# Optimization experiments

Hardware: AMD Instinct MI355X
Metric: run time of the kernel (lower is better)

## Reference

```python
import jax, jax.numpy as jnp
import numpy as np

B, N, C = 4, 1024, 512
H = 8
HD = C // H
SCALE = HD ** (-0.5)


def setup_inputs() -> dict:
    key = jax.random.key(0)
    ks = jax.random.split(key, 12)
    s = 0.02
    return {
        "x": jax.random.normal(ks[0], (B, N, C), dtype=jnp.float32),
        "y": jax.random.normal(ks[1], (B, N, C), dtype=jnp.float32),
        "Wqkv1": jax.random.normal(ks[2], (4 * C, C), dtype=jnp.float32) * s,
        "Wqkv2": jax.random.normal(ks[3], (4 * C, C), dtype=jnp.float32) * s,
        "W1": jax.random.normal(ks[4], (C, C), dtype=jnp.float32) * s,
        "b1": jnp.zeros((C,), dtype=jnp.float32),
        "W2": jax.random.normal(ks[5], (C, C), dtype=jnp.float32) * s,
        "b2": jnp.zeros((C,), dtype=jnp.float32),
        "W3": jax.random.normal(ks[6], (C, C), dtype=jnp.float32) * s,
        "b3": jnp.zeros((C,), dtype=jnp.float32),
        "W4": jax.random.normal(ks[7], (C, C), dtype=jnp.float32) * s,
        "b4": jnp.zeros((C,), dtype=jnp.float32),
    }


def _l2norm(t, eps=1e-12):
    # matches F.normalize(dim=-1)
    n = jnp.sqrt(jnp.sum(t * t, axis=-1, keepdims=True))
    return t / jnp.maximum(n, eps)


def _ortho_loss(q, qt):
    # q, qt: [B, H, N, HD]
    qn = _l2norm(q)
    qtn = _l2norm(qt)
    prod = jnp.einsum("bhnd,bhmd->bhnm", qn, qtn)  # [B,H,N,N]
    eye = jnp.eye(N, dtype=prod.dtype)
    off = prod * (1.0 - eye)
    # fro-norm squared of off-diagonal, divided by B*N*N (as in source)
    return jnp.sum(off * off) / (B * N * N)


def _qkv(inp, W):
    # inp: [B,N,C], W: [4C, C] -> [4, B, H, N, HD]
    t = (inp @ W.T).reshape(B, N, 4, H, HD)
    return jnp.transpose(t, (2, 0, 3, 1, 4))


def _attn(q, k, v):
    # q,k,v: [B,H,N,HD] -> [B,N,C]
    scores = jnp.einsum("bhnd,bhmd->bhnm", q, k) * SCALE
    a = jax.nn.softmax(scores, axis=-1)
    o = jnp.einsum("bhnm,bhmd->bhnd", a, v)
    return jnp.transpose(o, (0, 2, 1, 3)).reshape(B, N, C)


def reference(x, y, Wqkv1, Wqkv2, W1, b1, W2, b2, W3, b3, W4, b4):
    qkv1 = _qkv(x, Wqkv1)
    qkv2 = _qkv(y, Wqkv2)
    qx, kx, vx, qtx = qkv1[0], qkv1[1], qkv1[2], qkv1[3]
    qy, ky, vy, qty = qkv2[0], qkv2[1], qkv2[2], qkv2[3]

    lorthx = _ortho_loss(qx, qtx)
    lorthy = _ortho_loss(qy, qty)

    yc = _attn(qx, ky, vy)  # attncy @ vy
    xc = _attn(qy, kx, vx)  # attncx @ vx
    xt = _attn(qtx, kx, vx)
    yt = _attn(qty, ky, vy)

    xc = xc @ W1.T + b1
    yc = yc @ W2.T + b2
    xt = xt @ W3.T + b3
    yt = yt @ W4.T + b4

    # pairwise cosine distance between normalized xc, yc
    xcn = _l2norm(xc)
    ycn = _l2norm(yc)
    cos = jnp.sum(xcn * ycn, axis=-1)
    lc = jnp.mean(1.0 - cos)

    return (xc, yc, xt, yt, lorthx, lorthy, lc)
```

## Files before the change

### kernel.cpp

```cpp
#include <hip/hip_runtime.h>

typedef unsigned short u16;
typedef __attribute__((ext_vector_type(4))) unsigned short u16x4;
typedef __attribute__((ext_vector_type(8))) unsigned short u16x8;
typedef __attribute__((ext_vector_type(4))) float          f32x4;
typedef __attribute__((ext_vector_type(8))) __bf16         bf16x8;

#define MFMA16(a,b,c) __builtin_amdgcn_mfma_f32_16x16x32_bf16((a),(b),(c),0,0,0)
#define SCALE 0.125f
#define SCALE_LOG2E 0.18033688011112042f

__device__ __forceinline__ u16 f2b(float f){
  unsigned u = __builtin_bit_cast(unsigned, f);
  u = (u + 0x7fffu + ((u >> 16) & 1u)) >> 16;
  return (u16)u;
}
__device__ __forceinline__ u16 f2b_trunc(float f){
  return (u16)(__builtin_bit_cast(unsigned, f) >> 16);
}
__device__ __forceinline__ float b2f(u16 v){
  unsigned u = ((unsigned)v) << 16;
  return __builtin_bit_cast(float, u);
}
__device__ __forceinline__ void async16(const u16* g, u16* l){
  __builtin_amdgcn_global_load_lds(
      (const __attribute__((address_space(1))) unsigned*)g,
      (__attribute__((address_space(3))) unsigned*)l, 16, 0, 0);
}
__device__ __forceinline__ int swz(int row, int chunk, int off){
  return row*64 + (((chunk ^ row ^ (row >> 3)) & 7) << 3) + off;
}

__global__ void cast_all_k(const float* __restrict__ x, const float* __restrict__ y,
                           const float* __restrict__ wq1, const float* __restrict__ wq2,
                           const float* __restrict__ w1, const float* __restrict__ w2,
                           const float* __restrict__ w3, const float* __restrict__ w4,
                           u16* __restrict__ dst, float* __restrict__ outs){
  if (blockIdx.x == 0 && threadIdx.x < 3) outs[threadIdx.x] = 0.f;
  int i = blockIdx.x * 256 + threadIdx.x;
  const float* s; int base; float sc = 1.f;
  if      (i < 524288)  { s = x;   base = 0;       }
  else if (i < 1048576) { s = y;   base = 524288;  }
  else if (i < 1310720) { s = wq1; base = 1048576;
    int iw = i - base; if (iw < 65536 || iw >= 196608) sc = SCALE_LOG2E; }
  else if (i < 1572864) { s = wq2; base = 1310720;
    int iw = i - base; if (iw < 65536 || iw >= 196608) sc = SCALE_LOG2E; }
  else if (i < 1638400) { s = w1;  base = 1572864; }
  else if (i < 1703936) { s = w2;  base = 1638400; }
  else if (i < 1769472) { s = w3;  base = 1703936; }
  else                  { s = w4;  base = 1769472; }
  float4 v = ((const float4*)s)[i - base];
  u16x4 o; o[0]=f2b(v.x*sc); o[1]=f2b(v.y*sc); o[2]=f2b(v.z*sc); o[3]=f2b(v.w*sc);
  ((u16x4*)dst)[i] = o;
}

__global__ __launch_bounds__(256, 2) void qkv_mega_k(
    const u16* __restrict__ xb, const u16* __restrict__ Wq,
    u16* __restrict__ qkv, u16* __restrict__ vT)
{
  const int i = blockIdx.x;
  const u16 *A, *B; u16* C; int ldc, m0, n0;
  if (i < 512) {
    int z = i >> 8, t = i & 255;
    m0 = (t & 31)*128; n0 = (t >> 5)*128;
    A = xb + (size_t)z*2097152; B = Wq + (size_t)z*1048576;
    C = qkv + (size_t)z*8388608; ldc = 2048;
  } else if (i < 768) {
    int z = (i-512) >> 7, t = (i-512) & 127;
    m0 = (t & 31)*128; n0 = (t >> 5)*128;
    A = xb + (size_t)z*2097152; B = Wq + (size_t)z*1048576 + (size_t)1536*512;
    C = qkv + (size_t)z*8388608 + 1536; ldc = 2048;
  } else {
    int z = (i-768) >> 7, t = (i-768) & 127;
    m0 = (t & 3)*128; n0 = (t >> 2)*128;
    A = Wq + (size_t)z*1048576 + (size_t)1024*512; B = xb + (size_t)z*2097152;
    C = vT + (size_t)z*2097152; ldc = 4096;
  }

  __shared__ u16 As[128*32];
  __shared__ u16 Bs[128*32];
  const int tid  = threadIdx.x;
  const int w    = tid >> 6, lane = tid & 63;
  const int quad = lane >> 4, l16 = lane & 15;
  const int wr   = w >> 1, wc = w & 1;

  f32x4 acc[4][4] = {};
  const int rowa = lane >> 2;
  const int ko   = (lane & 3) * 8;

  for (int k0 = 0; k0 < 512; k0 += 32) {
    __syncthreads();
#pragma unroll
    for (int r = 0; r < 2; ++r) {
      int rb = (r*4 + w) * 16;
      async16(A + (size_t)(m0 + rb + rowa)*512 + k0 + ko, As + (r*4 + w)*512);
      async16(B + (size_t)(n0 + rb + rowa)*512 + k0 + ko, Bs + (r*4 + w)*512);
    }
    __syncthreads();
    bf16x8 af[4], bfr[4];
#pragma unroll
    for (int ii = 0; ii < 4; ++ii)
      af[ii] = *(const bf16x8*)&As[(wr*64 + ii*16 + l16)*32 + quad*8];
#pragma unroll
    for (int j = 0; j < 4; ++j)
      bfr[j] = *(const bf16x8*)&Bs[(wc*64 + j*16 + l16)*32 + quad*8];
#pragma unroll
    for (int ii = 0; ii < 4; ++ii)
#pragma unroll
      for (int j = 0; j < 4; ++j)
        acc[ii][j] = MFMA16(af[ii], bfr[j], acc[ii][j]);
  }
#pragma unroll
  for (int j = 0; j < 4; ++j) {
    int col = n0 + wc*64 + j*16 + l16;
#pragma unroll
    for (int ii = 0; ii < 4; ++ii)
#pragma unroll
      for (int reg = 0; reg < 4; ++reg) {
        int row = m0 + wr*64 + ii*16 + quad*4 + reg;
        C[(size_t)row*ldc + col] = f2b(acc[ii][j][reg]);
      }
  }
}

__global__ __launch_bounds__(256, 2) void gemm_fin_k(
    const u16* __restrict__ A0, size_t aStr, const u16* __restrict__ B0, size_t bStr,
    const float* __restrict__ bias0, const float* __restrict__ bias1,
    const float* __restrict__ bias2, const float* __restrict__ bias3,
    float* __restrict__ C0, size_t cStr,
    const float* __restrict__ Gbuf, float* __restrict__ outs)
{
  const int tid  = threadIdx.x;
  const int bid  = blockIdx.x;
  if (bid >= 512) {
    const int i = bid - 512;
    const int bh = i & 31, which = i >> 5;
    const float* base = Gbuf + (size_t)((which*32 + bh)*8) * 8192;
    float acc = 0.f;
    for (int idx = tid*4; idx < 4096; idx += 1024) {
      float4 gq = {0.f,0.f,0.f,0.f}, gt = {0.f,0.f,0.f,0.f};
#pragma unroll
      for (int t = 0; t < 8; ++t) {
        float4 a = *(const float4*)(base + (size_t)t*8192 + idx);
        float4 c = *(const float4*)(base + (size_t)t*8192 + 4096 + idx);
        gq.x += a.x; gq.y += a.y; gq.z += a.z; gq.w += a.w;
        gt.x += c.x; gt.y += c.y; gt.z += c.z; gt.w += c.w;
      }
      acc += gq.x*gt.x + gq.y*gt.y + gq.z*gt.z + gq.w*gt.w;
    }
    __shared__ float redsh[256];
    redsh[tid] = acc; __syncthreads();
    for (int s2 = 128; s2 > 0; s2 >>= 1) {
      if (tid < s2) redsh[tid] += redsh[tid + s2];
      __syncthreads();
    }
    if (tid == 0) atomicAdd(&outs[which], redsh[0] * (1.f/4194304.f));
    return;
  }

  const int z = bid >> 7, t7 = bid & 127;
  const int m0 = (t7 >> 2) * 128, n0 = (t7 & 3) * 128;
  const u16* A = A0 + (size_t)z * aStr;
  const u16* Bm = B0 + (size_t)z * bStr;
  float* Cb = C0 + (size_t)z * cStr;
  const float* bias = (z==0) ? bias0 : (z==1) ? bias1 : (z==2) ? bias2 : bias3;

  __shared__ u16 As[128*32];
  __shared__ u16 Bs[128*32];
  const int w    = tid >> 6, lane = tid & 63;
  const int quad = lane >> 4, l16 = lane & 15;
  const int wr   = w >> 1, wc = w & 1;

  f32x4 acc[4][4] = {};
  const int rowa = lane >> 2;
  const int ko   = (lane & 3) * 8;

  for (int k0 = 0; k0 < 512; k0 += 32) {
    __syncthreads();
#pragma unroll
    for (int r = 0; r < 2; ++r) {
      int rb = (r*4 + w) * 16;
      async16(A  + (size_t)(m0 + rb + rowa)*512 + k0 + ko, As + (r*4 + w)*512);
      async16(Bm + (size_t)(n0 + rb + rowa)*512 + k0 + ko, Bs + (r*4 + w)*512);
    }
    __syncthreads();
    bf16x8 af[4], bfr[4];
#pragma unroll
    for (int ii = 0; ii < 4; ++ii)
      af[ii] = *(const bf16x8*)&As[(wr*64 + ii*16 + l16)*32 + quad*8];
#pragma unroll
    for (int j = 0; j < 4; ++j)
      bfr[j] = *(const bf16x8*)&Bs[(wc*64 + j*16 + l16)*32 + quad*8];
#pragma unroll
    for (int ii = 0; ii < 4; ++ii)
#pragma unroll
      for (int j = 0; j < 4; ++j)
        acc[ii][j] = MFMA16(af[ii], bfr[j], acc[ii][j]);
  }
#pragma unroll
  for (int j = 0; j < 4; ++j) {
    int col = n0 + wc*64 + j*16 + l16;
    float bv = bias[col];
#pragma unroll
    for (int ii = 0; ii < 4; ++ii)
#pragma unroll
      for (int reg = 0; reg < 4; ++reg) {
        int row = m0 + wr*64 + ii*16 + quad*4 + reg;
        Cb[(size_t)row*512 + col] = acc[ii][j][reg] + bv;
      }
  }
}

__global__ __launch_bounds__(256, 2) void attn_ortho_k(
    const u16* __restrict__ qkv1, const u16* __restrict__ qkv2,
    const u16* __restrict__ vT1, const u16* __restrict__ vT2,
    u16* __restrict__ ao, float* __restrict__ Gbuf, float* __restrict__ outs)
{
  __shared__ u16 lds[24576];
  const int tid = threadIdx.x, w = tid >> 6, lane = tid & 63;
  const int quad = lane >> 4, l16 = lane & 15;

  if (blockIdx.x < 512) {
    u16* Ks = lds;
    u16* Vt = lds + 8192;
    u16* Ps = lds + 16384;

    const int lin = blockIdx.x;
    const int xcd = lin & 7, slot = lin >> 3;
    const int g   = xcd + 8*(slot >> 3);
    const int qt  = slot & 7;
    const int bh  = g >> 1, p = g & 1;
    const int b = bh >> 3, h = bh & 7;
    const u16* kvsrc = p ? qkv2 : qkv1;
    const u16* vsrc  = p ? vT2 : vT1;
    const u16* qsrcA = p ? qkv1 : qkv2;  const int qoffA = h*64;
    const u16* qsrcB = p ? qkv2 : qkv1;  const int qoffB = 1536 + h*64;
    const int koff = 512 + h*64;
    const size_t tb = (size_t)b * 1024;

    const int srow = tid >> 3, sch = tid & 7;

    u16x8 onesu;
#pragma unroll
    for (int ii = 0; ii < 8; ++ii) onesu[ii] = 0x3f80;
    const bf16x8 ONES = __builtin_bit_cast(bf16x8, onesu);

    bf16x8 qb[2][2][2];
#pragma unroll
    for (int s2 = 0; s2 < 2; ++s2) {
      size_t row = tb + qt*128 + w*32 + s2*16 + l16;
      const u16* qrA = qsrcA + row*2048 + qoffA;
      const u16* qrB = qsrcB + row*2048 + qoffB;
      qb[0][s2][0] = *(const bf16x8*)(qrA + quad*8);
      qb[0][s2][1] = *(const bf16x8*)(qrA + 32 + quad*8);
      qb[1][s2][0] = *(const bf16x8*)(qrB + quad*8);
      qb[1][s2][1] = *(const bf16x8*)(qrB + 32 + quad*8);
    }

    f32x4 oacc[2][2][4] = {};
    f32x4 lacc[2][2] = {};

    u16x8 kreg[2], vreg[2];
    auto loadTile = [&](int t){
#pragma unroll
      for (int r = 0; r < 2; ++r) {
        kreg[r] = *(const u16x8*)(kvsrc + (tb + t*64 + r*32 + srow)*2048 + koff + sch*8);
        vreg[r] = *(const u16x8*)(vsrc + (size_t)(h*64 + r*32 + srow)*4096 + tb + t*64 + sch*8);
      }
    };
    auto storeTile = [&](int buf){
#pragma unroll
      for (int r = 0; r < 2; ++r) {
        *(u16x8*)&Ks[buf*4096 + swz(r*32 + srow, sch, 0)] = kreg[r];
        *(u16x8*)&Vt[buf*4096 + swz(r*32 + srow, sch, 0)] = vreg[r];
      }
    };

    loadTile(0);
    storeTile(0);
    loadTile(1);

    for (int kt = 0; kt < 16; ++kt) {
      const int cur = kt & 1;
      __syncthreads();
      if (kt < 15) storeTile(cur ^ 1);
      if (kt < 14) loadTile(kt + 2);

      bf16x8 ka[4][2], vb[4][2];
#pragma unroll
      for (int j = 0; j < 4; ++j) {
        ka[j][0] = *(const bf16x8*)&Ks[cur*4096 + swz(j*16 + l16, quad, 0)];
        ka[j][1] = *(const bf16x8*)&Ks[cur*4096 + swz(j*16 + l16, quad + 4, 0)];
        vb[j][0] = *(const bf16x8*)&Vt[cur*4096 + swz(j*16 + l16, quad, 0)];
        vb[j][1] = *(const bf16x8*)&Vt[cur*4096 + swz(j*16 + l16, quad + 4, 0)];
      }

      bf16x8 paP0, paP1;
#pragma unroll
      for (int idx = 0; idx < 4; ++idx) {
        const int o = idx >> 1, s2 = idx & 1;
        u16* wP = Ps + w*2048 + (idx & 1)*1024;
        f32x4 t[4];
        __builtin_amdgcn_s_setprio(1);
#pragma unroll
        for (int j = 0; j < 4; ++j) {
          f32x4 z = {};
          z    = MFMA16(ka[j][0], qb[o][s2][0], z);
          t[j] = MFMA16(ka[j][1], qb[o][s2][1], z);
        }
        __builtin_amdgcn_s_setprio(0);
        if (idx > 0) {
          const u16* rP = Ps + w*2048 + ((idx - 1) & 1)*1024;
          paP0 = *(const bf16x8*)&rP[swz(l16, quad, 0)];
          paP1 = *(const bf16x8*)&rP[swz(l16, quad + 4, 0)];
        }
#pragma unroll
        for (int j = 0; j < 4; ++j) {
          u16x4 pk;
#pragma unroll
          for (int reg = 0; reg < 4; ++reg)
            pk[reg] = f2b_trunc(__builtin_amdgcn_exp2f(t[j][reg]));
          *(u16x4*)&wP[swz(l16, j*2 + (quad >> 1), (quad & 1)*4)] = pk;
        }
        if (idx > 0) {
          const int po = (idx - 1) >> 1, ps2 = (idx - 1) & 1;
          __builtin_amdgcn_s_setprio(1);
#pragma unroll
          for (int j = 0; j < 4; ++j) {
            oacc[po][ps2][j] = MFMA16(paP0, vb[j][0], oacc[po][ps2][j]);
            oacc[po][ps2][j] = MFMA16(paP1, vb[j][1], oacc[po][ps2][j]);
          }
          lacc[po][ps2] = MFMA16(paP0, ONES, lacc[po][ps2]);
          lacc[po][ps2] = MFMA16(paP1, ONES, lacc[po][ps2]);
          __builtin_amdgcn_s_setprio(0);
        }
      }
      {
        const u16* rP = Ps + w*2048 + 1024;
        bf16x8 pa0 = *(const bf16x8*)&rP[swz(l16, quad, 0)];
        bf16x8 pa1 = *(const bf16x8*)&rP[swz(l16, quad + 4, 0)];
        __builtin_amdgcn_s_setprio(1);
#pragma unroll
        for (int j = 0; j < 4; ++j) {
          oacc[1][1][j] = MFMA16(pa0, vb[j][0], oacc[1][1][j]);
          oacc[1][1][j] = MFMA16(pa1, vb[j][1], oacc[1][1][j]);
        }
        lacc[1][1] = MFMA16(pa0, ONES, lacc[1][1]);
        lacc[1][1] = MFMA16(pa1, ONES, lacc[1][1]);
        __builtin_amdgcn_s_setprio(0);
      }
    }

#pragma unroll
    for (int o = 0; o < 2; ++o) {
      int a = p + o*2;
      u16* aop = ao + (size_t)a*(4096*512) + (tb + qt*128)*512 + h*64;
#pragma unroll
      for (int s2 = 0; s2 < 2; ++s2) {
#pragma unroll
        for (int reg = 0; reg < 4; ++reg) {
          float linv = 1.f / lacc[o][s2][reg];
          int row = w*32 + s2*16 + quad*4 + reg;
#pragma unroll
          for (int j = 0; j < 4; ++j)
            aop[(size_t)row*512 + j*16 + l16] = f2b(oacc[o][s2][j][reg] * linv);
        }
      }
    }
  } else {
    u16* QnT  = lds;
    u16* QtnT = lds + 4096;

    const int i = blockIdx.x - 512;
    const int bh = i & 31, which = (i >> 5) & 1, tg = i >> 6;
    const u16* src = which ? qkv2 : qkv1;
    const int b = bh >> 3, h = bh & 7;
    const size_t tb = (size_t)b * 1024;

    f32x4 gq[4] = {}, gqt[4] = {};
    float diag = 0.f;

    for (int tt = 0; tt < 2; ++tt) {
      int t = tg*2 + tt;
      __syncthreads();
      if (tid < 128) {
        int tok = tid & 63, mat = tid >> 6;
        const u16* pp = src + (tb + t*64 + tok)*2048 + (mat ? 1536 : 0) + h*64;
        u16x8 rowv[8];
#pragma unroll
        for (int ii = 0; ii < 8; ++ii) rowv[ii] = *(const u16x8*)(pp + ii*8);
        float ss = 0.f;
#pragma unroll
        for (int ii = 0; ii < 8; ++ii)
#pragma unroll
          for (int jj = 0; jj < 8; ++jj) { float f = b2f(rowv[ii][jj]); ss += f*f; }
        float inv = 1.f / fmaxf(sqrtf(ss), 1e-12f);
        u16* dst = mat ? QtnT : QnT;
#pragma unroll
        for (int ii = 0; ii < 8; ++ii)
#pragma unroll
          for (int jj = 0; jj < 8; ++jj)
            dst[swz(ii*8 + jj, tok >> 3, tok & 7)] = f2b(b2f(rowv[ii][jj]) * inv);
        if (mat == 0) {
          const u16* p2 = src + (tb + t*64 + tok)*2048 + 1536 + h*64;
          float ss2 = 0.f, dot = 0.f;
#pragma unroll
          for (int ii = 0; ii < 8; ++ii) {
            u16x8 r2 = *(const u16x8*)(p2 + ii*8);
#pragma unroll
            for (int jj = 0; jj < 8; ++jj) {
              float fq = b2f(rowv[ii][jj]), ft = b2f(r2[jj]);
              ss2 += ft*ft; dot += fq*ft;
            }
          }
          float inv2 = 1.f / fmaxf(sqrtf(ss2), 1e-12f);
          float dn = dot * inv * inv2;
          diag += dn * dn;
        }
      }
      __syncthreads();
      bf16x8 a0 = *(const bf16x8*)&QnT [swz(w*16 + l16, quad, 0)];
      bf16x8 a1 = *(const bf16x8*)&QnT [swz(w*16 + l16, quad + 4, 0)];
      bf16x8 t0 = *(const bf16x8*)&QtnT[swz(w*16 + l16, quad, 0)];
      bf16x8 t1 = *(const bf16x8*)&QtnT[swz(w*16 + l16, quad + 4, 0)];
#pragma unroll
      for (int j = 0; j < 4; ++j) {
        bf16x8 b0 = *(const bf16x8*)&QnT [swz(j*16 + l16, quad, 0)];
        bf16x8 b1 = *(const bf16x8*)&QnT [swz(j*16 + l16, quad + 4, 0)];
        gq[j]  = MFMA16(a0, b0, gq[j]);
        gq[j]  = MFMA16(a1, b1, gq[j]);
        bf16x8 c0 = *(const bf16x8*)&QtnT[swz(j*16 + l16, quad, 0)];
        bf16x8 c1 = *(const bf16x8*)&QtnT[swz(j*16 + l16, quad + 4, 0)];
        gqt[j] = MFMA16(t0, c0, gqt[j]);
        gqt[j] = MFMA16(t1, c1, gqt[j]);
      }
    }
    float* Gq = Gbuf + (size_t)((which*32 + bh)*8 + tg) * 8192;
    float* Gt = Gq + 4096;
#pragma unroll
    for (int j = 0; j < 4; ++j)
#pragma unroll
      for (int reg = 0; reg < 4; ++reg) {
        int row = w*16 + quad*4 + reg, col = j*16 + l16;
        Gq[row*64 + col] = gq[j][reg];
        Gt[row*64 + col] = gqt[j][reg];
      }
    if (tid < 64) {
#pragma unroll
      for (int off = 32; off > 0; off >>= 1) diag += __shfl_xor(diag, off);
      if (tid == 0) atomicAdd(&outs[which], -diag * (1.f/4194304.f));
    }
  }
}

__global__ __launch_bounds__(256, 2) void red_k(
    const float* __restrict__ dout, float* __restrict__ outs)
{
  const int tid = threadIdx.x;
  const int w = tid >> 6, lane = tid & 63;
  const int wid = blockIdx.x * 4 + w;
  float acc = 0.f;
  for (int rr = 0; rr < 16; ++rr) {
    int row = wid*16 + rr;
    const float4* xr = (const float4*)(dout + (size_t)row*512 + lane*8);
    const float4* yr = (const float4*)(dout + 2097152 + (size_t)row*512 + lane*8);
    float4 x0 = xr[0], x1 = xr[1], y0 = yr[0], y1 = yr[1];
    float dxy = x0.x*y0.x + x0.y*y0.y + x0.z*y0.z + x0.w*y0.w
              + x1.x*y1.x + x1.y*y1.y + x1.z*y1.z + x1.w*y1.w;
    float sx  = x0.x*x0.x + x0.y*x0.y + x0.z*x0.z + x0.w*x0.w
              + x1.x*x1.x + x1.y*x1.y + x1.z*x1.z + x1.w*x1.w;
    float sy  = y0.x*y0.x + y0.y*y0.y + y0.z*y0.z + y0.w*y0.w
              + y1.x*y1.x + y1.y*y1.y + y1.z*y1.z + y1.w*y1.w;
#pragma unroll
    for (int off = 32; off > 0; off >>= 1) {
      dxy += __shfl_xor(dxy, off);
      sx  += __shfl_xor(sx,  off);
      sy  += __shfl_xor(sy,  off);
    }
    if (lane == 0) {
      float cosv = dxy / (fmaxf(sqrtf(sx), 1e-12f) * fmaxf(sqrtf(sy), 1e-12f));
      acc += 1.f - cosv;
    }
  }
  if (lane == 0) atomicAdd(&outs[2], acc * (1.f/4096.f));
}

extern "C" void kernel_launch(void* const* d_in, const int* in_sizes, int n_in,
                              void* d_out, int out_size, void* d_ws, size_t ws_size,
                              hipStream_t stream)
{
  (void)in_sizes; (void)n_in; (void)out_size; (void)ws_size;
  const float* x     = (const float*)d_in[0];
  const float* y     = (const float*)d_in[1];
  const float* Wqkv1 = (const float*)d_in[2];
  const float* Wqkv2 = (const float*)d_in[3];
  const float* W1 = (const float*)d_in[4];
  const float* b1 = (const float*)d_in[5];
  const float* W2 = (const float*)d_in[6];
  const float* b2 = (const float*)d_in[7];
  const float* W3 = (const float*)d_in[8];
  const float* b3 = (const float*)d_in[9];
  const float* W4 = (const float*)d_in[10];
  const float* b4 = (const float*)d_in[11];

  u16* ws   = (u16*)d_ws;
  u16* xb   = ws;
  u16* Wq1b = ws + (size_t)4194304;
  u16* W1b  = ws + (size_t)6291456;
  u16* qkv1 = ws + (size_t)7340032;
  u16* qkv2 = qkv1 + (size_t)8388608;
  u16* aob  = qkv2 + (size_t)8388608;
  float* Gbuf = (float*)(aob + (size_t)8388608);
  u16* vT1 = (u16*)d_out;
  u16* vT2 = vT1 + (size_t)2097152;

  float* outb = (float*)d_out;
  float* outs = outb + 8388608;

  cast_all_k<<<dim3(7168), dim3(256), 0, stream>>>(
      x, y, Wqkv1, Wqkv2, W1, W2, W3, W4, xb, outs);

  qkv_mega_k<<<dim3(1024), dim3(256), 0, stream>>>(xb, Wq1b, qkv1, vT1);

  attn_ortho_k<<<dim3(1024), 256, 0, stream>>>(qkv1, qkv2, vT1, vT2, aob, Gbuf, outs);

  gemm_fin_k<<<dim3(576), 256, 0, stream>>>(
      aob, 2097152, W1b, 262144, b1, b2, b3, b4, outb, 2097152, Gbuf, outs);

  red_k<<<dim3(64), 256, 0, stream>>>(outb, outs);
}
```

Measured before the change: 213.8 us.

## Double attention block size to 512 threads sharing K/V tiles across 256 query rows

Attention blocks now use 512 threads (8 waves) and each covers 256 query rows instead of 128, halving the number of attention blocks. Each K/V tile loaded into LDS is reused by twice as many query rows, and each thread loads one row-chunk instead of two. Ortho blocks are packed two-per-block, each half using its own LDS region. This cuts redundant K/V global traffic but raises LDS use and changes occupancy; launch bounds of 512x4 may pressure registers.

```diff
diff --git a/kernel.cpp b/kernel.cpp
--- a/kernel.cpp
+++ b/kernel.cpp
@@ -211,24 +211,26 @@
   }
 }
 
-__global__ __launch_bounds__(256, 2) void attn_ortho_k(
+__global__ __launch_bounds__(512, 4) void attn_ortho_k(
     const u16* __restrict__ qkv1, const u16* __restrict__ qkv2,
     const u16* __restrict__ vT1, const u16* __restrict__ vT2,
     u16* __restrict__ ao, float* __restrict__ Gbuf, float* __restrict__ outs)
 {
-  __shared__ u16 lds[24576];
-  const int tid = threadIdx.x, w = tid >> 6, lane = tid & 63;
-  const int quad = lane >> 4, l16 = lane & 15;
-
-  if (blockIdx.x < 512) {
+  __shared__ u16 lds[32768];
+  const int tid = threadIdx.x;
+
+  if (blockIdx.x < 256) {
     u16* Ks = lds;
     u16* Vt = lds + 8192;
     u16* Ps = lds + 16384;
 
+    const int w = tid >> 6, lane = tid & 63;
+    const int quad = lane >> 4, l16 = lane & 15;
+
     const int lin = blockIdx.x;
     const int xcd = lin & 7, slot = lin >> 3;
-    const int g   = xcd + 8*(slot >> 3);
-    const int qt  = slot & 7;
+    const int g   = xcd + 8*(slot >> 2);
+    const int qt  = slot & 3;
     const int bh  = g >> 1, p = g & 1;
     const int b = bh >> 3, h = bh & 7;
     const u16* kvsrc = p ? qkv2 : qkv1;
@@ -248,7 +250,7 @@
     bf16x8 qb[2][2][2];
 #pragma unroll
     for (int s2 = 0; s2 < 2; ++s2) {
-      size_t row = tb + qt*128 + w*32 + s2*16 + l16;
+      size_t row = tb + qt*256 + w*32 + s2*16 + l16;
       const u16* qrA = qsrcA + row*2048 + qoffA;
       const u16* qrB = qsrcB + row*2048 + qoffB;
       qb[0][s2][0] = *(const bf16x8*)(qrA + quad*8);
@@ -260,20 +262,14 @@
     f32x4 oacc[2][2][4] = {};
     f32x4 lacc[2][2] = {};
 
-    u16x8 kreg[2], vreg[2];
+    u16x8 kreg, vreg;
     auto loadTile = [&](int t){
-#pragma unroll
-      for (int r = 0; r < 2; ++r) {
-        kreg[r] = *(const u16x8*)(kvsrc + (tb + t*64 + r*32 + srow)*2048 + koff + sch*8);
-        vreg[r] = *(const u16x8*)(vsrc + (size_t)(h*64 + r*32 + srow)*4096 + tb + t*64 + sch*8);
-      }
+      kreg = *(const u16x8*)(kvsrc + (tb + t*64 + srow)*2048 + koff + sch*8);
+      vreg = *(const u16x8*)(vsrc + (size_t)(h*64 + srow)*4096 + tb + t*64 + sch*8);
     };
     auto storeTile = [&](int buf){
-#pragma unroll
-      for (int r = 0; r < 2; ++r) {
-        *(u16x8*)&Ks[buf*4096 + swz(r*32 + srow, sch, 0)] = kreg[r];
-        *(u16x8*)&Vt[buf*4096 + swz(r*32 + srow, sch, 0)] = vreg[r];
-      }
+      *(u16x8*)&Ks[buf*4096 + swz(srow, sch, 0)] = kreg;
+      *(u16x8*)&Vt[buf*4096 + swz(srow, sch, 0)] = vreg;
     };
 
     loadTile(0);
@@ -354,7 +350,7 @@
 #pragma unroll
     for (int o = 0; o < 2; ++o) {
       int a = p + o*2;
-      u16* aop = ao + (size_t)a*(4096*512) + (tb + qt*128)*512 + h*64;
+      u16* aop = ao + (size_t)a*(4096*512) + (tb + qt*256)*512 + h*64;
 #pragma unroll
       for (int s2 = 0; s2 < 2; ++s2) {
 #pragma unroll
@@ -368,11 +364,15 @@
       }
     }
   } else {
-    u16* QnT  = lds;
-    u16* QtnT = lds + 4096;
-
-    const int i = blockIdx.x - 512;
+    const int h2 = tid >> 8, htid = tid & 255;
+    const int hw = htid >> 6, hlane = htid & 63;
+    const int hquad = hlane >> 4, hl16 = hlane & 15;
+    u16* QnT  = lds + h2*8192;
+    u16* QtnT = lds + h2*8192 + 4096;
+
+    const int i = blockIdx.x - 256;
     const int bh = i & 31, which = (i >> 5) & 1, tg = i >> 6;
+    const int s = tg*2 + h2;
     const u16* src = which ? qkv2 : qkv1;
     const int b = bh >> 3, h = bh & 7;
     const size_t tb = (size_t)b * 1024;
@@ -381,10 +381,10 @@
     float diag = 0.f;
 
     for (int tt = 0; tt < 2; ++tt) {
-      int t = tg*2 + tt;
+      int t = s*2 + tt;
       __syncthreads();
-      if (tid < 128) {
-        int tok = tid & 63, mat = tid >> 6;
+      if (htid < 128) {
+        int tok = htid & 63, mat = htid >> 6;
         const u16* pp = src + (tb + t*64 + tok)*2048 + (mat ? 1536 : 0) + h*64;
         u16x8 rowv[8];
 #pragma unroll
@@ -419,36 +419,36 @@
         }
       }
       __syncthreads();
-      bf16x8 a0 = *(const bf16x8*)&QnT [swz(w*16 + l16, quad, 0)];
-      bf16x8 a1 = *(const bf16x8*)&QnT [swz(w*16 + l16, quad + 4, 0)];
-      bf16x8 t0 = *(const bf16x8*)&QtnT[swz(w*16 + l16, quad, 0)];
-      bf16x8 t1 = *(const bf16x8*)&QtnT[swz(w*16 + l16, quad + 4, 0)];
+      bf16x8 a0 = *(const bf16x8*)&QnT [swz(hw*16 + hl16, hquad, 0)];
+      bf16x8 a1 = *(const bf16x8*)&QnT [swz(hw*16 + hl16, hquad + 4, 0)];
+      bf16x8 t0 = *(const bf16x8*)&QtnT[swz(hw*16 + hl16, hquad, 0)];
+      bf16x8 t1 = *(const bf16x8*)&QtnT[swz(hw*16 + hl16, hquad + 4, 0)];
 #pragma unroll
       for (int j = 0; j < 4; ++j) {
-        bf16x8 b0 = *(const bf16x8*)&QnT [swz(j*16 + l16, quad, 0)];
-        bf16x8 b1 = *(const bf16x8*)&QnT [swz(j*16 + l16, quad + 4, 0)];
+        bf16x8 b0 = *(const bf16x8*)&QnT [swz(j*16 + hl16, hquad, 0)];
+        bf16x8 b1 = *(const bf16x8*)&QnT [swz(j*16 + hl16, hquad + 4, 0)];
         gq[j]  = MFMA16(a0, b0, gq[j]);
         gq[j]  = MFMA16(a1, b1, gq[j]);
-        bf16x8 c0 = *(const bf16x8*)&QtnT[swz(j*16 + l16, quad, 0)];
-        bf16x8 c1 = *(const bf16x8*)&QtnT[swz(j*16 + l16, quad + 4, 0)];
+        bf16x8 c0 = *(const bf16x8*)&QtnT[swz(j*16 + hl16, hquad, 0)];
+        bf16x8 c1 = *(const bf16x8*)&QtnT[swz(j*16 + hl16, hquad + 4, 0)];
         gqt[j] = MFMA16(t0, c0, gqt[j]);
         gqt[j] = MFMA16(t1, c1, gqt[j]);
       }
     }
-    float* Gq = Gbuf + (size_t)((which*32 + bh)*8 + tg) * 8192;
+    float* Gq = Gbuf + (size_t)((which*32 + bh)*8 + s) * 8192;
     float* Gt = Gq + 4096;
 #pragma unroll
     for (int j = 0; j < 4; ++j)
 #pragma unroll
       for (int reg = 0; reg < 4; ++reg) {
-        int row = w*16 + quad*4 + reg, col = j*16 + l16;
+        int row = hw*16 + hquad*4 + reg, col = j*16 + hl16;
         Gq[row*64 + col] = gq[j][reg];
         Gt[row*64 + col] = gqt[j][reg];
       }
-    if (tid < 64) {
+    if (htid < 64) {
 #pragma unroll
       for (int off = 32; off > 0; off >>= 1) diag += __shfl_xor(diag, off);
-      if (tid == 0) atomicAdd(&outs[which], -diag * (1.f/4194304.f));
+      if (htid == 0) atomicAdd(&outs[which], -diag * (1.f/4194304.f));
     }
   }
 }
@@ -522,7 +522,7 @@
 
   qkv_mega_k<<<dim3(1024), dim3(256), 0, stream>>>(xb, Wq1b, qkv1, vT1);
 
-  attn_ortho_k<<<dim3(1024), 256, 0, stream>>>(qkv1, qkv2, vT1, vT2, aob, Gbuf, outs);
+  attn_ortho_k<<<dim3(512), 512, 0, stream>>>(qkv1, qkv2, vT1, vT2, aob, Gbuf, outs);
 
   gemm_fin_k<<<dim3(576), 256, 0, stream>>>(
       aob, 2097152, W1b, 262144, b1, b2, b3, b4, outb, 2097152, Gbuf, outs);
```

Measured after the change: 394.6 us. +84.5%, slower.
